# Kernel tuning notes

Hardware: AMD Instinct MI355X
Metric: run time of the kernel (lower is better)

## Reference

```python
import jax, jax.numpy as jnp
import numpy as np

SEQ, B, D_IN, D_H = 4096, 256, 64, 128


def setup_inputs() -> dict:
    key = jax.random.key(0)
    k1, k2, k3, k4, k5 = jax.random.split(key, 5)
    return {
        "input": jax.random.normal(k1, (SEQ, B, D_IN), dtype=jnp.float32),
        "W_ih": jax.random.normal(k2, (D_H, D_IN), dtype=jnp.float32) * (1.0 / np.sqrt(D_IN)),
        "b_ih": jax.random.normal(k3, (D_H,), dtype=jnp.float32) * 0.02,
        "W_hh": jax.random.normal(k4, (D_H, D_H), dtype=jnp.float32) * (1.0 / np.sqrt(D_H)),
        "b_hh": jax.random.normal(k5, (D_H,), dtype=jnp.float32) * 0.02,
    }


def reference(input, W_ih, b_ih, W_hh, b_hh):
    # Precompute input projections for all steps in one big GEMM: [S,B,128]
    x_proj = jnp.einsum('sbi,hi->sbh', input, W_ih) + b_ih + b_hh

    def step(h, x_t):
        # h: [B,128]; tanh(ih(x_t) + hh(h))
        h_new = jnp.tanh(x_t + h @ W_hh.T)
        return h_new, None

    h0 = jnp.zeros((input.shape[1], W_hh.shape[0]), dtype=input.dtype)
    h_final, _ = jax.lax.scan(step, h0, x_proj)
    return h_final  # [B,128]
```

## Files before the change

### kernel.cpp

```cpp
#include <hip/hip_runtime.h>


#define SEQ   4096
#define BATCH 256
#define DIN   64
#define DH    128
#define XSTEP (BATCH * DIN)

typedef _Float16 half8  __attribute__((ext_vector_type(8)));
typedef _Float16 half4v __attribute__((ext_vector_type(4)));
typedef _Float16 half2v __attribute__((ext_vector_type(2)));
typedef __fp16   fp16x2 __attribute__((ext_vector_type(2)));
typedef float    f32x4  __attribute__((ext_vector_type(4)));
typedef float    f32x2  __attribute__((ext_vector_type(2)));

union H2 { fp16x2 q; half2v h; unsigned int u; };

__device__ __forceinline__ float fast_tanh(float v) {
    float e = __builtin_amdgcn_exp2f(v * 2.88539008177792681472f);
    return 1.0f - 2.0f * __builtin_amdgcn_rcpf(e + 1.0f);
}

__device__ __forceinline__ half2v pk(float a, float b) {
    H2 u; u.q = __builtin_amdgcn_cvt_pkrtz(a, b);
    return u.h;
}

__device__ __forceinline__ half8 cvt8(f32x4 a, f32x4 b) {
    half2v p0 = pk(a[0], a[1]);
    half2v p1 = pk(a[2], a[3]);
    half2v p2 = pk(b[0], b[1]);
    half2v p3 = pk(b[2], b[3]);
    half8 r;
    r[0] = p0[0]; r[1] = p0[1]; r[2] = p1[0]; r[3] = p1[1];
    r[4] = p2[0]; r[5] = p2[1]; r[6] = p3[0]; r[7] = p3[1];
    return r;
}

__device__ __forceinline__ half4v pack4(f32x4 a) {
    half2v q0 = pk(a[0], a[1]);
    half2v q1 = pk(a[2], a[3]);
    half4v r;
    r[0] = q0[0]; r[1] = q0[1]; r[2] = q1[0]; r[3] = q1[1];
    return r;
}

__device__ __forceinline__ f32x4 cvt4f(half4v v) {
    f32x4 r;
    r[0] = (float)v[0]; r[1] = (float)v[1];
    r[2] = (float)v[2]; r[3] = (float)v[3];
    return r;
}

__device__ __forceinline__ int hoff(int b, int j) {
    return b * 256 + ((((j >> 3) ^ b) & 15) << 4) + (j & 7) * 2;
}

__launch_bounds__(256, 1)
__global__ void rnn_prepass(const float* __restrict__ x,
                            const float* __restrict__ Wih,
                            const float* __restrict__ bih,
                            const float* __restrict__ bhh,
                            _Float16* __restrict__ xp)
{
    const int tid  = threadIdx.x;
    const int w    = tid >> 6;
    const int lane = tid & 63;
    const int lb   = lane & 15;
    const int lg   = lane >> 4;
    const int rowbase = blockIdx.x * 64 + w * 16;

    half8 A[8][2];
    #pragma unroll
    for (int s = 0; s < 8; ++s) {
        #pragma unroll
        for (int kt = 0; kt < 2; ++kt) {
            const float* wr = Wih + (s * 16 + lb) * DIN + kt * 32 + lg * 8;
            half8 f;
            #pragma unroll
            for (int i = 0; i < 8; ++i) f[i] = (_Float16)wr[i];
            A[s][kt] = f;
        }
    }
    f32x4 bias[8];
    #pragma unroll
    for (int s = 0; s < 8; ++s)
        #pragma unroll
        for (int r = 0; r < 4; ++r) {
            int j = s * 16 + lg * 4 + r;
            bias[s][r] = bih[j] + bhh[j];
        }

    const float* xr = x + (size_t)(rowbase + lb) * DIN + lg * 8;
    half8 xf0 = cvt8(*(const f32x4*)(xr),      *(const f32x4*)(xr + 4));
    half8 xf1 = cvt8(*(const f32x4*)(xr + 32), *(const f32x4*)(xr + 36));

    _Float16* op = xp + (size_t)(rowbase + lb) * DH + lg * 4;
    #pragma unroll
    for (int s = 0; s < 8; ++s) {
        f32x4 acc;
        acc = __builtin_amdgcn_mfma_f32_16x16x32_f16(A[s][0], xf0, bias[s], 0, 0, 0);
        acc = __builtin_amdgcn_mfma_f32_16x16x32_f16(A[s][1], xf1, acc,     0, 0, 0);
        *(half4v*)(op + s * 16) = pack4(acc);
    }
}

__launch_bounds__(512, 1)
__global__ void rnn_scan_xp(const _Float16* __restrict__ xp,
                            const float* __restrict__ Whh,
                            float* __restrict__ out)
{
    __shared__ __align__(16) char hbuf[8192];

    const int tid   = threadIdx.x;
    const int wave  = tid >> 6;
    const int lane  = tid & 63;
    const int lb    = lane & 15;
    const int lg    = lane >> 4;
    const int bbase = blockIdx.x << 4;
    const int jbase = wave << 4;

    half8 Ahh[4];
    #pragma unroll
    for (int kt = 0; kt < 4; ++kt) {
        const float* wr = Whh + (jbase + lb) * DH + kt * 32 + lg * 8;
        half8 f;
        #pragma unroll
        for (int i = 0; i < 8; ++i) f[i] = (_Float16)wr[i];
        Ahh[kt] = f;
    }

    const _Float16* xpp = xp + (size_t)(bbase + lb) * DH + jbase + (lg << 2);
    const size_t XPS = (size_t)BATCH * DH;

    half4v xq1, xq2, xq3;
    f32x4 ci;
    {
        half4v x0 = *(const half4v*)(xpp);
        xq1 = *(const half4v*)(xpp + 1 * XPS);
        xq2 = *(const half4v*)(xpp + 2 * XPS);
        xq3 = *(const half4v*)(xpp + 3 * XPS);
        ci = cvt4f(x0);
    }
    const _Float16* xload = xpp + 4 * XPS;

    half8 hf0, hf1, hf2, hf3;
    {
        half8 z;
        #pragma unroll
        for (int i = 0; i < 8; ++i) z[i] = (_Float16)0.0f;
        hf0 = hf1 = hf2 = hf3 = z;
    }

    const int woff  = hoff(lb, jbase + (lg << 2));
    const int roff0 = hoff(lb, 0 * 32 + (lg << 3));
    const int roff1 = hoff(lb, 1 * 32 + (lg << 3));
    const int roff2 = hoff(lb, 2 * 32 + (lg << 3));
    const int roff3 = hoff(lb, 3 * 32 + (lg << 3));

    #pragma unroll 2
    for (int t = 0; t < SEQ - 1; ++t) {
        const int nb = (t + 1) & 1;
        char* hb = hbuf + nb * 4096;

        f32x4 zz = {0.0f, 0.0f, 0.0f, 0.0f};
        f32x4 acc1, acc2;
        acc1 = __builtin_amdgcn_mfma_f32_16x16x32_f16(Ahh[0], hf0, ci,   0, 0, 0);
        acc2 = __builtin_amdgcn_mfma_f32_16x16x32_f16(Ahh[2], hf2, zz,   0, 0, 0);
        acc1 = __builtin_amdgcn_mfma_f32_16x16x32_f16(Ahh[1], hf1, acc1, 0, 0, 0);
        acc2 = __builtin_amdgcn_mfma_f32_16x16x32_f16(Ahh[3], hf3, acc2, 0, 0, 0);

        half4v xnew = *(const half4v*)xload;
        if (t + 5 < SEQ) xload += XPS;

        f32x4 rA;
        #pragma unroll
        for (int r = 0; r < 4; ++r) rA[r] = fast_tanh(acc1[r] + acc2[r]);
        *(half4v*)(hb + woff) = pack4(rA);

        ci = cvt4f(xq1);
        xq1 = xq2; xq2 = xq3; xq3 = xnew;

        asm volatile("s_waitcnt lgkmcnt(0)" ::: "memory");
        __builtin_amdgcn_s_barrier();
        asm volatile("" ::: "memory");

        hf0 = *(const half8*)(hb + roff0);
        hf2 = *(const half8*)(hb + roff2);
        hf1 = *(const half8*)(hb + roff1);
        hf3 = *(const half8*)(hb + roff3);
    }

    {
        f32x4 zz = {0.0f, 0.0f, 0.0f, 0.0f};
        f32x4 acc1, acc2;
        acc1 = __builtin_amdgcn_mfma_f32_16x16x32_f16(Ahh[0], hf0, ci,   0, 0, 0);
        acc2 = __builtin_amdgcn_mfma_f32_16x16x32_f16(Ahh[2], hf2, zz,   0, 0, 0);
        acc1 = __builtin_amdgcn_mfma_f32_16x16x32_f16(Ahh[1], hf1, acc1, 0, 0, 0);
        acc2 = __builtin_amdgcn_mfma_f32_16x16x32_f16(Ahh[3], hf3, acc2, 0, 0, 0);
        f32x4 rA;
        #pragma unroll
        for (int r = 0; r < 4; ++r) rA[r] = fast_tanh(acc1[r] + acc2[r]);
        *(f32x4*)(out + (size_t)(bbase + lb) * DH + jbase + (lg << 2)) = rA;
    }
}

__device__ __forceinline__ int hoffc(int b, int chunk, int lo) {
    return b * 256 + ((chunk ^ b) << 4) + lo;
}
__device__ __forceinline__ int xoff_lds(int b, int chunk, int lo) {
    return b * 128 + (((chunk ^ (b & 7)) << 4) + lo);
}

__launch_bounds__(512, 1)
__global__ void rnn_fused_scan_r2(const float* __restrict__ x,
                                  const float* __restrict__ Wih,
                                  const float* __restrict__ bih,
                                  const float* __restrict__ Whh,
                                  const float* __restrict__ bhh,
                                  float* __restrict__ out)
{
    __shared__ __align__(16) char lds[12288];
    char* hbuf = lds;
    char* xbuf = lds + 8192;

    const int tid   = threadIdx.x;
    const int wave  = tid >> 6;
    const int lane  = tid & 63;
    const int lb    = lane & 15;
    const int lg    = lane >> 4;
    const int bbase = blockIdx.x << 4;
    const int jbase = wave << 4;

    half8 Ahh[4], Aih[2];
    #pragma unroll
    for (int kt = 0; kt < 4; ++kt) {
        const float* wr = Whh + (jbase + lb) * DH + kt * 32 + lg * 8;
        half8 f;
        #pragma unroll
        for (int i = 0; i < 8; ++i) f[i] = (_Float16)wr[i];
        Ahh[kt] = f;
    }
    #pragma unroll
    for (int kt = 0; kt < 2; ++kt) {
        const float* wr = Wih + (jbase + lb) * DIN + kt * 32 + lg * 8;
        half8 f;
        #pragma unroll
        for (int i = 0; i < 8; ++i) f[i] = (_Float16)wr[i];
        Aih[kt] = f;
    }
    f32x4 bias;
    #pragma unroll
    for (int r = 0; r < 4; ++r) {
        int j = jbase + lg * 4 + r;
        bias[r] = bih[j] + bhh[j];
    }

    const int bx = tid >> 5;
    const int kx = (tid & 31) << 1;
    const float* xlane = x + (size_t)(bbase + bx) * DIN + kx;

    f32x2 r0  = *(const f32x2*)(xlane + 0 * (size_t)XSTEP);
    f32x2 rx0 = *(const f32x2*)(xlane + 1 * (size_t)XSTEP);
    f32x2 rx1 = *(const f32x2*)(xlane + 2 * (size_t)XSTEP);
    f32x2 rx2 = *(const f32x2*)(xlane + 3 * (size_t)XSTEP);
    {
        half2v p; p[0] = (_Float16)r0[0]; p[1] = (_Float16)r0[1];
        *(half2v*)(xbuf + xoff_lds(bx, kx >> 3, (kx & 7) * 2)) = p;
    }
    const float* xload = xlane + 4 * (size_t)XSTEP;

    half8 hf0, hf1, hf2, hf3, xf0, xf1;
    {
        half8 z;
        #pragma unroll
        for (int i = 0; i < 8; ++i) z[i] = (_Float16)0.0f;
        hf0 = hf1 = hf2 = hf3 = z;
    }

    asm volatile("s_waitcnt lgkmcnt(0)" ::: "memory");
    __builtin_amdgcn_s_barrier();
    asm volatile("" ::: "memory");
    xf0 = *(const half8*)(xbuf + xoff_lds(lb, 0 * 4 + lg, 0));
    xf1 = *(const half8*)(xbuf + xoff_lds(lb, 1 * 4 + lg, 0));

    f32x4 acc_ih;
    acc_ih = __builtin_amdgcn_mfma_f32_16x16x32_f16(Aih[0], xf0, bias,   0, 0, 0);
    acc_ih = __builtin_amdgcn_mfma_f32_16x16x32_f16(Aih[1], xf1, acc_ih, 0, 0, 0);

    #pragma unroll 2
    for (int t = 0; t < SEQ - 1; ++t) {
        f32x4 zz = {0.0f, 0.0f, 0.0f, 0.0f};
        f32x4 acc1, acc2;
        acc1 = __builtin_amdgcn_mfma_f32_16x16x32_f16(Ahh[0], hf0, acc_ih, 0, 0, 0);
        acc2 = __builtin_amdgcn_mfma_f32_16x16x32_f16(Ahh[2], hf2, zz,     0, 0, 0);
        acc1 = __builtin_amdgcn_mfma_f32_16x16x32_f16(Ahh[1], hf1, acc1,   0, 0, 0);
        acc2 = __builtin_amdgcn_mfma_f32_16x16x32_f16(Ahh[3], hf3, acc2,   0, 0, 0);

        const int nb = (t + 1) & 1;
        {
            half2v p; p[0] = (_Float16)rx0[0]; p[1] = (_Float16)rx0[1];
            *(half2v*)(xbuf + nb * 2048 + xoff_lds(bx, kx >> 3, (kx & 7) * 2)) = p;
        }
        rx0 = rx1; rx1 = rx2;
        rx2 = *(const f32x2*)xload;
        if (t + 5 < SEQ) xload += XSTEP;

        f32x4 hv;
        #pragma unroll
        for (int r = 0; r < 4; ++r) hv[r] = fast_tanh(acc1[r] + acc2[r]);
        {
            half4v p;
            #pragma unroll
            for (int r = 0; r < 4; ++r) p[r] = (_Float16)hv[r];
            *(half4v*)(hbuf + nb * 4096 + hoffc(lb, (wave << 1) + (lg >> 1), (lg & 1) * 8)) = p;
        }

        asm volatile("s_waitcnt lgkmcnt(0)" ::: "memory");
        __builtin_amdgcn_s_barrier();
        asm volatile("" ::: "memory");

        hf0 = *(const half8*)(hbuf + nb * 4096 + hoffc(lb, 0 * 4 + lg, 0));
        hf2 = *(const half8*)(hbuf + nb * 4096 + hoffc(lb, 2 * 4 + lg, 0));
        hf1 = *(const half8*)(hbuf + nb * 4096 + hoffc(lb, 1 * 4 + lg, 0));
        hf3 = *(const half8*)(hbuf + nb * 4096 + hoffc(lb, 3 * 4 + lg, 0));
        xf0 = *(const half8*)(xbuf + nb * 2048 + xoff_lds(lb, 0 * 4 + lg, 0));
        xf1 = *(const half8*)(xbuf + nb * 2048 + xoff_lds(lb, 1 * 4 + lg, 0));

        acc_ih = __builtin_amdgcn_mfma_f32_16x16x32_f16(Aih[0], xf0, bias,   0, 0, 0);
        acc_ih = __builtin_amdgcn_mfma_f32_16x16x32_f16(Aih[1], xf1, acc_ih, 0, 0, 0);
    }

    {
        f32x4 zz = {0.0f, 0.0f, 0.0f, 0.0f};
        f32x4 acc1, acc2;
        acc1 = __builtin_amdgcn_mfma_f32_16x16x32_f16(Ahh[0], hf0, acc_ih, 0, 0, 0);
        acc2 = __builtin_amdgcn_mfma_f32_16x16x32_f16(Ahh[2], hf2, zz,     0, 0, 0);
        acc1 = __builtin_amdgcn_mfma_f32_16x16x32_f16(Ahh[1], hf1, acc1,   0, 0, 0);
        acc2 = __builtin_amdgcn_mfma_f32_16x16x32_f16(Ahh[3], hf3, acc2,   0, 0, 0);
        f32x4 res;
        #pragma unroll
        for (int r = 0; r < 4; ++r) res[r] = fast_tanh(acc1[r] + acc2[r]);
        *(f32x4*)(out + (size_t)(bbase + lb) * DH + jbase + (lg << 2)) = res;
    }
}

extern "C" void kernel_launch(void* const* d_in, const int* in_sizes, int n_in,
                              void* d_out, int out_size, void* d_ws, size_t ws_size,
                              hipStream_t stream) {
    const float* x   = (const float*)d_in[0];
    const float* Wih = (const float*)d_in[1];
    const float* bih = (const float*)d_in[2];
    const float* Whh = (const float*)d_in[3];
    const float* bhh = (const float*)d_in[4];
    float* out = (float*)d_out;

    const size_t need = (size_t)SEQ * BATCH * DH * sizeof(_Float16);
    if (ws_size >= need) {
        _Float16* xp = (_Float16*)d_ws;
        rnn_prepass<<<SEQ * BATCH / 64, 256, 0, stream>>>(x, Wih, bih, bhh, xp);
        rnn_scan_xp<<<16, 512, 0, stream>>>(xp, Whh, out);
    } else {
        rnn_fused_scan_r2<<<16, 512, 0, stream>>>(x, Wih, bih, Whh, bhh, out);
    }
}
```

Baseline: 1.424 ms.

## Fuse input projection into scan with producer waves and per-block global ring

Replaces the separate prepass GEMM kernel plus scan kernel with one kernel of 768 threads per block. Four low-priority producer waves compute the input projection 64 steps ahead into a per-block global ring buffer, and eight high-priority consumer waves run the recurrence, reading x_proj from the ring. This removes the full-size intermediate write/read and the second launch, and overlaps projection work with the latency-bound scan. The cost is that every timestep now carries a block-wide barrier shared with the producers. Ring visibility relies on barriers and vmcnt waits rather than explicit fences.

```diff
diff --git a/kernel.cpp b/kernel.cpp
--- a/kernel.cpp
+++ b/kernel.cpp
@@ -5,7 +5,10 @@
 #define BATCH 256
 #define DIN   64
 #define DH    128
-#define XSTEP (BATCH * DIN)
+#define LEAD   64
+#define RSLOTS 128
+#define SLOT_BYTES 4096
+#define RING_BYTES ((size_t)RSLOTS * SLOT_BYTES)
 
 typedef _Float16 half8  __attribute__((ext_vector_type(8)));
 typedef _Float16 half4v __attribute__((ext_vector_type(4)));
@@ -19,6 +22,10 @@
 __device__ __forceinline__ float fast_tanh(float v) {
     float e = __builtin_amdgcn_exp2f(v * 2.88539008177792681472f);
     return 1.0f - 2.0f * __builtin_amdgcn_rcpf(e + 1.0f);
+}
+
+__device__ __forceinline__ int hoff(int b, int j) {
+    return b * 256 + ((((j >> 3) ^ b) & 15) << 4) + (j & 7) * 2;
 }
 
 __device__ __forceinline__ half2v pk(float a, float b) {
@@ -52,63 +59,23 @@
     return r;
 }
 
-__device__ __forceinline__ int hoff(int b, int j) {
-    return b * 256 + ((((j >> 3) ^ b) & 15) << 4) + (j & 7) * 2;
-}
-
-__launch_bounds__(256, 1)
-__global__ void rnn_prepass(const float* __restrict__ x,
-                            const float* __restrict__ Wih,
-                            const float* __restrict__ bih,
-                            const float* __restrict__ bhh,
-                            _Float16* __restrict__ xp)
-{
-    const int tid  = threadIdx.x;
-    const int w    = tid >> 6;
-    const int lane = tid & 63;
-    const int lb   = lane & 15;
-    const int lg   = lane >> 4;
-    const int rowbase = blockIdx.x * 64 + w * 16;
-
-    half8 A[8][2];
-    #pragma unroll
-    for (int s = 0; s < 8; ++s) {
-        #pragma unroll
-        for (int kt = 0; kt < 2; ++kt) {
-            const float* wr = Wih + (s * 16 + lb) * DIN + kt * 32 + lg * 8;
-            half8 f;
-            #pragma unroll
-            for (int i = 0; i < 8; ++i) f[i] = (_Float16)wr[i];
-            A[s][kt] = f;
-        }
-    }
-    f32x4 bias[8];
-    #pragma unroll
-    for (int s = 0; s < 8; ++s)
-        #pragma unroll
-        for (int r = 0; r < 4; ++r) {
-            int j = s * 16 + lg * 4 + r;
-            bias[s][r] = bih[j] + bhh[j];
-        }
-
-    const float* xr = x + (size_t)(rowbase + lb) * DIN + lg * 8;
-    half8 xf0 = cvt8(*(const f32x4*)(xr),      *(const f32x4*)(xr + 4));
-    half8 xf1 = cvt8(*(const f32x4*)(xr + 32), *(const f32x4*)(xr + 36));
-
-    _Float16* op = xp + (size_t)(rowbase + lb) * DH + lg * 4;
-    #pragma unroll
-    for (int s = 0; s < 8; ++s) {
-        f32x4 acc;
-        acc = __builtin_amdgcn_mfma_f32_16x16x32_f16(A[s][0], xf0, bias[s], 0, 0, 0);
-        acc = __builtin_amdgcn_mfma_f32_16x16x32_f16(A[s][1], xf1, acc,     0, 0, 0);
-        *(half4v*)(op + s * 16) = pack4(acc);
-    }
-}
-
-__launch_bounds__(512, 1)
-__global__ void rnn_scan_xp(const _Float16* __restrict__ xp,
-                            const float* __restrict__ Whh,
-                            float* __restrict__ out)
+struct XSlot { f32x4 v0, v1, v2, v3; };
+
+#define XLOAD(slot, p_) do {                                           \
+        (slot).v0 = *(const f32x4*)(p_);                               \
+        (slot).v1 = *(const f32x4*)((p_) + 4);                         \
+        (slot).v2 = *(const f32x4*)((p_) + 32);                        \
+        (slot).v3 = *(const f32x4*)((p_) + 36);                        \
+    } while (0)
+
+__launch_bounds__(768, 3)
+__global__ void rnn_fused_all(const float* __restrict__ x,
+                              const float* __restrict__ Wih,
+                              const float* __restrict__ bih,
+                              const float* __restrict__ Whh,
+                              const float* __restrict__ bhh,
+                              float* __restrict__ out,
+                              char* __restrict__ ring_all)
 {
     __shared__ __align__(16) char hbuf[8192];
 
@@ -118,93 +85,147 @@
     const int lb    = lane & 15;
     const int lg    = lane >> 4;
     const int bbase = blockIdx.x << 4;
-    const int jbase = wave << 4;
-
-    half8 Ahh[4];
-    #pragma unroll
-    for (int kt = 0; kt < 4; ++kt) {
-        const float* wr = Whh + (jbase + lb) * DH + kt * 32 + lg * 8;
-        half8 f;
-        #pragma unroll
-        for (int i = 0; i < 8; ++i) f[i] = (_Float16)wr[i];
-        Ahh[kt] = f;
-    }
-
-    const _Float16* xpp = xp + (size_t)(bbase + lb) * DH + jbase + (lg << 2);
-    const size_t XPS = (size_t)BATCH * DH;
-
-    half4v xq1, xq2, xq3;
-    f32x4 ci;
-    {
-        half4v x0 = *(const half4v*)(xpp);
-        xq1 = *(const half4v*)(xpp + 1 * XPS);
-        xq2 = *(const half4v*)(xpp + 2 * XPS);
-        xq3 = *(const half4v*)(xpp + 3 * XPS);
-        ci = cvt4f(x0);
-    }
-    const _Float16* xload = xpp + 4 * XPS;
-
-    half8 hf0, hf1, hf2, hf3;
-    {
-        half8 z;
-        #pragma unroll
-        for (int i = 0; i < 8; ++i) z[i] = (_Float16)0.0f;
-        hf0 = hf1 = hf2 = hf3 = z;
-    }
-
-    const int woff  = hoff(lb, jbase + (lg << 2));
-    const int roff0 = hoff(lb, 0 * 32 + (lg << 3));
-    const int roff1 = hoff(lb, 1 * 32 + (lg << 3));
-    const int roff2 = hoff(lb, 2 * 32 + (lg << 3));
-    const int roff3 = hoff(lb, 3 * 32 + (lg << 3));
-
-    #pragma unroll 2
-    for (int t = 0; t < SEQ - 1; ++t) {
-        const int nb = (t + 1) & 1;
-        char* hb = hbuf + nb * 4096;
-
-        f32x4 zz = {0.0f, 0.0f, 0.0f, 0.0f};
-        f32x4 acc1, acc2;
-        acc1 = __builtin_amdgcn_mfma_f32_16x16x32_f16(Ahh[0], hf0, ci,   0, 0, 0);
-        acc2 = __builtin_amdgcn_mfma_f32_16x16x32_f16(Ahh[2], hf2, zz,   0, 0, 0);
-        acc1 = __builtin_amdgcn_mfma_f32_16x16x32_f16(Ahh[1], hf1, acc1, 0, 0, 0);
-        acc2 = __builtin_amdgcn_mfma_f32_16x16x32_f16(Ahh[3], hf3, acc2, 0, 0, 0);
-
-        half4v xnew = *(const half4v*)xload;
-        if (t + 5 < SEQ) xload += XPS;
-
-        f32x4 rA;
-        #pragma unroll
-        for (int r = 0; r < 4; ++r) rA[r] = fast_tanh(acc1[r] + acc2[r]);
-        *(half4v*)(hb + woff) = pack4(rA);
-
-        ci = cvt4f(xq1);
-        xq1 = xq2; xq2 = xq3; xq3 = xnew;
-
-        asm volatile("s_waitcnt lgkmcnt(0)" ::: "memory");
-        __builtin_amdgcn_s_barrier();
-        asm volatile("" ::: "memory");
-
-        hf0 = *(const half8*)(hb + roff0);
-        hf2 = *(const half8*)(hb + roff2);
-        hf1 = *(const half8*)(hb + roff1);
-        hf3 = *(const half8*)(hb + roff3);
-    }
-
-    {
-        f32x4 zz = {0.0f, 0.0f, 0.0f, 0.0f};
-        f32x4 acc1, acc2;
-        acc1 = __builtin_amdgcn_mfma_f32_16x16x32_f16(Ahh[0], hf0, ci,   0, 0, 0);
-        acc2 = __builtin_amdgcn_mfma_f32_16x16x32_f16(Ahh[2], hf2, zz,   0, 0, 0);
-        acc1 = __builtin_amdgcn_mfma_f32_16x16x32_f16(Ahh[1], hf1, acc1, 0, 0, 0);
-        acc2 = __builtin_amdgcn_mfma_f32_16x16x32_f16(Ahh[3], hf3, acc2, 0, 0, 0);
-        f32x4 rA;
-        #pragma unroll
-        for (int r = 0; r < 4; ++r) rA[r] = fast_tanh(acc1[r] + acc2[r]);
-        *(f32x4*)(out + (size_t)(bbase + lb) * DH + jbase + (lg << 2)) = rA;
-    }
-}
-
+    char* ring = ring_all + (size_t)blockIdx.x * RING_BYTES;
+
+    if (wave < 8) {
+        __builtin_amdgcn_s_setprio(1);
+        const int jbase = wave << 4;
+
+        half8 Ahh[4];
+        #pragma unroll
+        for (int kt = 0; kt < 4; ++kt) {
+            const float* wr = Whh + (jbase + lb) * DH + kt * 32 + (lg << 3);
+            half8 f;
+            #pragma unroll
+            for (int i = 0; i < 8; ++i) f[i] = (_Float16)wr[i];
+            Ahh[kt] = f;
+        }
+        f32x4 biasv;
+        #pragma unroll
+        for (int r = 0; r < 4; ++r) {
+            int j = jbase + (lg << 2) + r;
+            biasv[r] = bih[j] + bhh[j];
+        }
+
+        const int woff  = hoff(lb, jbase + (lg << 2));
+        const int roff0 = hoff(lb, 0 * 32 + (lg << 3));
+        const int roff1 = hoff(lb, 1 * 32 + (lg << 3));
+        const int roff2 = hoff(lb, 2 * 32 + (lg << 3));
+        const int roff3 = hoff(lb, 3 * 32 + (lg << 3));
+        const int rdoff = lb * 256 + ((jbase + (lg << 2)) << 1);
+
+        half8 hf0, hf1, hf2, hf3;
+        {
+            half8 z;
+            #pragma unroll
+            for (int i = 0; i < 8; ++i) z[i] = (_Float16)0.0f;
+            hf0 = hf1 = hf2 = hf3 = z;
+        }
+        f32x4 ci = {0.0f, 0.0f, 0.0f, 0.0f};
+        half4v xq1 = {};
+
+        #pragma unroll 2
+        for (int s = -LEAD; s < SEQ - 1; ++s) {
+            if (s >= 0) {
+                const int t = s;
+                char* hb = hbuf + (((t + 1) & 1) << 12);
+
+                f32x4 zz = {0.0f, 0.0f, 0.0f, 0.0f};
+                f32x4 acc1, acc2;
+                acc1 = __builtin_amdgcn_mfma_f32_16x16x32_f16(Ahh[0], hf0, ci,   0, 0, 0);
+                acc2 = __builtin_amdgcn_mfma_f32_16x16x32_f16(Ahh[2], hf2, zz,   0, 0, 0);
+                acc1 = __builtin_amdgcn_mfma_f32_16x16x32_f16(Ahh[1], hf1, acc1, 0, 0, 0);
+                acc2 = __builtin_amdgcn_mfma_f32_16x16x32_f16(Ahh[3], hf3, acc2, 0, 0, 0);
+
+                const int tn = (t + 2 < SEQ) ? t + 2 : SEQ - 1;
+                half4v xnew = *(const half4v*)(ring + ((tn & (RSLOTS - 1)) * SLOT_BYTES) + rdoff);
+
+                f32x4 rA;
+                #pragma unroll
+                for (int r = 0; r < 4; ++r) rA[r] = fast_tanh(acc1[r] + acc2[r]);
+                *(half4v*)(hb + woff) = pack4(rA);
+
+                ci = cvt4f(xq1) + biasv;
+                xq1 = xnew;
+
+                asm volatile("s_waitcnt lgkmcnt(0)" ::: "memory");
+                __builtin_amdgcn_s_barrier();
+                asm volatile("" ::: "memory");
+
+                hf0 = *(const half8*)(hb + roff0);
+                hf2 = *(const half8*)(hb + roff2);
+                hf1 = *(const half8*)(hb + roff1);
+                hf3 = *(const half8*)(hb + roff3);
+            } else {
+                __builtin_amdgcn_s_barrier();
+                asm volatile("" ::: "memory");
+                if (s == -1) {
+                    half4v x0 = *(const half4v*)(ring + 0 * SLOT_BYTES + rdoff);
+                    xq1       = *(const half4v*)(ring + 1 * SLOT_BYTES + rdoff);
+                    ci = cvt4f(x0) + biasv;
+                }
+            }
+        }
+
+        {
+            f32x4 zz = {0.0f, 0.0f, 0.0f, 0.0f};
+            f32x4 acc1, acc2;
+            acc1 = __builtin_amdgcn_mfma_f32_16x16x32_f16(Ahh[0], hf0, ci,   0, 0, 0);
+            acc2 = __builtin_amdgcn_mfma_f32_16x16x32_f16(Ahh[2], hf2, zz,   0, 0, 0);
+            acc1 = __builtin_amdgcn_mfma_f32_16x16x32_f16(Ahh[1], hf1, acc1, 0, 0, 0);
+            acc2 = __builtin_amdgcn_mfma_f32_16x16x32_f16(Ahh[3], hf3, acc2, 0, 0, 0);
+            f32x4 rA;
+            #pragma unroll
+            for (int r = 0; r < 4; ++r) rA[r] = fast_tanh(acc1[r] + acc2[r]);
+            *(f32x4*)(out + (size_t)(bbase + lb) * DH + jbase + (lg << 2)) = rA;
+        }
+    } else {
+        __builtin_amdgcn_s_setprio(0);
+        const int h = wave - 8;
+
+        half8 Aih[8][2];
+        #pragma unroll
+        for (int s8 = 0; s8 < 8; ++s8) {
+            #pragma unroll
+            for (int kt = 0; kt < 2; ++kt) {
+                const float* wr = Wih + (s8 * 16 + lb) * DIN + kt * 32 + (lg << 3);
+                half8 f;
+                #pragma unroll
+                for (int i = 0; i < 8; ++i) f[i] = (_Float16)wr[i];
+                Aih[s8][kt] = f;
+            }
+        }
+
+        XSlot xs;
+        XLOAD(xs, x + ((size_t)h * BATCH + bbase + lb) * DIN + (lg << 3));
+
+        for (int s = -LEAD; s < SEQ - 1; ++s) {
+            const int tp = s + LEAD;
+            if ((tp & 3) == h && tp < SEQ) {
+                half8 xf0 = cvt8(xs.v0, xs.v1);
+                half8 xf1 = cvt8(xs.v2, xs.v3);
+                char* wp = ring + ((tp & (RSLOTS - 1)) * SLOT_BYTES) + lb * 256 + (lg << 3);
+                f32x4 zz = {0.0f, 0.0f, 0.0f, 0.0f};
+                #pragma unroll
+                for (int s8 = 0; s8 < 8; ++s8) {
+                    f32x4 a;
+                    a = __builtin_amdgcn_mfma_f32_16x16x32_f16(Aih[s8][0], xf0, zz, 0, 0, 0);
+                    a = __builtin_amdgcn_mfma_f32_16x16x32_f16(Aih[s8][1], xf1, a,  0, 0, 0);
+                    *(half4v*)(wp + s8 * 32) = pack4(a);
+                }
+                const int tl = tp + 4;
+                if (tl < SEQ) {
+                    XLOAD(xs, x + ((size_t)tl * BATCH + bbase + lb) * DIN + (lg << 3));
+                }
+                asm volatile("s_waitcnt vmcnt(4)" ::: "memory");
+            }
+            __builtin_amdgcn_s_barrier();
+            asm volatile("" ::: "memory");
+        }
+    }
+}
+
+#define XSTEP (BATCH * DIN)
 __device__ __forceinline__ int hoffc(int b, int chunk, int lo) {
     return b * 256 + ((chunk ^ b) << 4) + lo;
 }
@@ -355,11 +376,9 @@
     const float* bhh = (const float*)d_in[4];
     float* out = (float*)d_out;
 
-    const size_t need = (size_t)SEQ * BATCH * DH * sizeof(_Float16);
+    const size_t need = 16 * RING_BYTES;
     if (ws_size >= need) {
-        _Float16* xp = (_Float16*)d_ws;
-        rnn_prepass<<<SEQ * BATCH / 64, 256, 0, stream>>>(x, Wih, bih, bhh, xp);
-        rnn_scan_xp<<<16, 512, 0, stream>>>(xp, Whh, out);
+        rnn_fused_all<<<16, 768, 0, stream>>>(x, Wih, bih, Whh, bhh, out, (char*)d_ws);
     } else {
         rnn_fused_scan_r2<<<16, 512, 0, stream>>>(x, Wih, bih, Whh, bhh, out);
     }
```

New measurement: 2.765 ms. 94.1% more time.

## Overlap input projection with recurrent scan via producer-consumer persistent kernel

Applied to the files above, without the earlier changes.

Replaces the separate prepass and scan launches with one 80-block kernel. Sixteen blocks run the recurrent scan, and 64 producer blocks compute the fp16 input projection per batch group. Producers publish progress through atomic ready counters that consumers poll before each 32-step chunk. This hides the projection GEMM time behind the serial scan. In exchange it adds a memset launch, polling overhead, and depends on producer and consumer blocks being co-resident to avoid deadlock.

```diff
diff --git a/kernel.cpp b/kernel.cpp
--- a/kernel.cpp
+++ b/kernel.cpp
@@ -6,6 +6,7 @@
 #define DIN   64
 #define DH    128
 #define XSTEP (BATCH * DIN)
+#define XP_BYTES ((size_t)SEQ * BATCH * DH * 2)
 
 typedef _Float16 half8  __attribute__((ext_vector_type(8)));
 typedef _Float16 half4v __attribute__((ext_vector_type(4)));
@@ -56,7 +57,206 @@
     return b * 256 + ((((j >> 3) ^ b) & 15) << 4) + (j & 7) * 2;
 }
 
-__launch_bounds__(256, 1)
+struct XSlot { f32x4 v0, v1, v2, v3; };
+#define XLOAD(slot, p_) do {                                           \
+        (slot).v0 = *(const f32x4*)(p_);                               \
+        (slot).v1 = *(const f32x4*)((p_) + 4);                         \
+        (slot).v2 = *(const f32x4*)((p_) + 32);                        \
+        (slot).v3 = *(const f32x4*)((p_) + 36);                        \
+    } while (0)
+
+__device__ __forceinline__ void pollwait(const int* rdy, int tgt) {
+    for (;;) {
+        int r0 = __hip_atomic_load(rdy + 0, __ATOMIC_ACQUIRE, __HIP_MEMORY_SCOPE_AGENT);
+        int r1 = __hip_atomic_load(rdy + 1, __ATOMIC_ACQUIRE, __HIP_MEMORY_SCOPE_AGENT);
+        int r2 = __hip_atomic_load(rdy + 2, __ATOMIC_ACQUIRE, __HIP_MEMORY_SCOPE_AGENT);
+        int r3 = __hip_atomic_load(rdy + 3, __ATOMIC_ACQUIRE, __HIP_MEMORY_SCOPE_AGENT);
+        int m = r0 < r1 ? r0 : r1;
+        int n = r2 < r3 ? r2 : r3;
+        if (n < m) m = n;
+        if (4 * m >= tgt) return;
+        __builtin_amdgcn_s_sleep(8);
+    }
+}
+
+__launch_bounds__(512, 1)
+__global__ void rnn_pc(const float* __restrict__ x,
+                       const float* __restrict__ Wih,
+                       const float* __restrict__ bih,
+                       const float* __restrict__ Whh,
+                       const float* __restrict__ bhh,
+                       float* __restrict__ out,
+                       _Float16* __restrict__ xp,
+                       int* __restrict__ ready)
+{
+    __shared__ __align__(16) char hbuf[8192];
+
+    const int tid  = threadIdx.x;
+    const int wave = tid >> 6;
+    const int lane = tid & 63;
+    const int lb   = lane & 15;
+    const int lg   = lane >> 4;
+
+    if (blockIdx.x < 16) {
+        const int g     = blockIdx.x;
+        const int bbase = g << 4;
+        const int jbase = wave << 4;
+        const int* rdy  = ready + g * 4;
+
+        half8 Ahh[4];
+        #pragma unroll
+        for (int kt = 0; kt < 4; ++kt) {
+            const float* wr = Whh + (jbase + lb) * DH + kt * 32 + (lg << 3);
+            half8 f;
+            #pragma unroll
+            for (int i = 0; i < 8; ++i) f[i] = (_Float16)wr[i];
+            Ahh[kt] = f;
+        }
+
+        pollwait(rdy, 8);
+
+        const _Float16* xpp = xp + (size_t)(bbase + lb) * DH + jbase + (lg << 2);
+        const size_t XPS = (size_t)BATCH * DH;
+
+        half4v xq1, xq2, xq3;
+        f32x4 ci;
+        {
+            half4v x0 = *(const half4v*)(xpp);
+            xq1 = *(const half4v*)(xpp + 1 * XPS);
+            xq2 = *(const half4v*)(xpp + 2 * XPS);
+            xq3 = *(const half4v*)(xpp + 3 * XPS);
+            ci = cvt4f(x0);
+        }
+        const _Float16* xload = xpp + 4 * XPS;
+
+        half8 hf0, hf1, hf2, hf3;
+        {
+            half8 z;
+            #pragma unroll
+            for (int i = 0; i < 8; ++i) z[i] = (_Float16)0.0f;
+            hf0 = hf1 = hf2 = hf3 = z;
+        }
+
+        const int woff  = hoff(lb, jbase + (lg << 2));
+        const int roff0 = hoff(lb, 0 * 32 + (lg << 3));
+        const int roff1 = hoff(lb, 1 * 32 + (lg << 3));
+        const int roff2 = hoff(lb, 2 * 32 + (lg << 3));
+        const int roff3 = hoff(lb, 3 * 32 + (lg << 3));
+
+        #define SCAN_BODY(T_) do {                                                   \
+            const int t_ = (T_);                                                     \
+            char* hb = hbuf + (((t_ + 1) & 1) << 12);                                \
+            f32x4 zz = {0.0f, 0.0f, 0.0f, 0.0f};                                     \
+            f32x4 acc1, acc2;                                                        \
+            acc1 = __builtin_amdgcn_mfma_f32_16x16x32_f16(Ahh[0], hf0, ci,   0,0,0); \
+            acc2 = __builtin_amdgcn_mfma_f32_16x16x32_f16(Ahh[2], hf2, zz,   0,0,0); \
+            acc1 = __builtin_amdgcn_mfma_f32_16x16x32_f16(Ahh[1], hf1, acc1, 0,0,0); \
+            acc2 = __builtin_amdgcn_mfma_f32_16x16x32_f16(Ahh[3], hf3, acc2, 0,0,0); \
+            half4v xnew = *(const half4v*)xload;                                     \
+            if (t_ + 5 < SEQ) xload += XPS;                                          \
+            f32x4 rA;                                                                \
+            _Pragma("unroll")                                                        \
+            for (int r = 0; r < 4; ++r) rA[r] = fast_tanh(acc1[r] + acc2[r]);        \
+            *(half4v*)(hb + woff) = pack4(rA);                                       \
+            ci = cvt4f(xq1);                                                         \
+            xq1 = xq2; xq2 = xq3; xq3 = xnew;                                        \
+            asm volatile("s_waitcnt lgkmcnt(0)" ::: "memory");                       \
+            __builtin_amdgcn_s_barrier();                                            \
+            asm volatile("" ::: "memory");                                           \
+            hf0 = *(const half8*)(hb + roff0);                                       \
+            hf2 = *(const half8*)(hb + roff2);                                       \
+            hf1 = *(const half8*)(hb + roff1);                                       \
+            hf3 = *(const half8*)(hb + roff3);                                       \
+        } while (0)
+
+        for (int T = 0; T < 4064; T += 32) {
+            pollwait(rdy, T + 36);
+            #pragma unroll 2
+            for (int tt = 0; tt < 32; ++tt) SCAN_BODY(T + tt);
+        }
+        pollwait(rdy, 4096);
+        #pragma unroll 2
+        for (int t = 4064; t < 4095; ++t) SCAN_BODY(t);
+
+        {
+            f32x4 zz = {0.0f, 0.0f, 0.0f, 0.0f};
+            f32x4 acc1, acc2;
+            acc1 = __builtin_amdgcn_mfma_f32_16x16x32_f16(Ahh[0], hf0, ci,   0, 0, 0);
+            acc2 = __builtin_amdgcn_mfma_f32_16x16x32_f16(Ahh[2], hf2, zz,   0, 0, 0);
+            acc1 = __builtin_amdgcn_mfma_f32_16x16x32_f16(Ahh[1], hf1, acc1, 0, 0, 0);
+            acc2 = __builtin_amdgcn_mfma_f32_16x16x32_f16(Ahh[3], hf3, acc2, 0, 0, 0);
+            f32x4 rA;
+            #pragma unroll
+            for (int r = 0; r < 4; ++r) rA[r] = fast_tanh(acc1[r] + acc2[r]);
+            *(f32x4*)(out + (size_t)(bbase + lb) * DH + jbase + (lg << 2)) = rA;
+        }
+        #undef SCAN_BODY
+    } else {
+        const int p  = blockIdx.x - 16;
+        const int g  = p >> 2;
+        const int q  = p & 3;
+        const int bb = g << 4;
+
+        half8 A[8][2];
+        #pragma unroll
+        for (int s = 0; s < 8; ++s) {
+            #pragma unroll
+            for (int kt = 0; kt < 2; ++kt) {
+                const float* wr = Wih + (s * 16 + lb) * DIN + kt * 32 + (lg << 3);
+                half8 f;
+                #pragma unroll
+                for (int i = 0; i < 8; ++i) f[i] = (_Float16)wr[i];
+                A[s][kt] = f;
+            }
+        }
+        f32x4 bias[8];
+        #pragma unroll
+        for (int s = 0; s < 8; ++s)
+            #pragma unroll
+            for (int r = 0; r < 4; ++r) {
+                int j = s * 16 + (lg << 2) + r;
+                bias[s][r] = bih[j] + bhh[j];
+            }
+
+        XSlot xs;
+        {
+            int t0 = q + (wave << 2);
+            XLOAD(xs, x + ((size_t)t0 * BATCH + bb + lb) * DIN + (lg << 3));
+        }
+
+        for (int i = 0; i < 128; ++i) {
+            const int t = q + ((((i << 3) + wave)) << 2);
+
+            half8 xf0 = cvt8(xs.v0, xs.v1);
+            half8 xf1 = cvt8(xs.v2, xs.v3);
+
+            XSlot xn;
+            if (i + 1 < 128) {
+                int tn = q + (((((i + 1) << 3) + wave)) << 2);
+                XLOAD(xn, x + ((size_t)tn * BATCH + bb + lb) * DIN + (lg << 3));
+            }
+
+            _Float16* op = xp + ((size_t)t * BATCH + bb + lb) * DH + (lg << 2);
+            #pragma unroll
+            for (int s = 0; s < 8; ++s) {
+                f32x4 acc;
+                acc = __builtin_amdgcn_mfma_f32_16x16x32_f16(A[s][0], xf0, bias[s], 0, 0, 0);
+                acc = __builtin_amdgcn_mfma_f32_16x16x32_f16(A[s][1], xf1, acc,     0, 0, 0);
+                *(half4v*)(op + s * 16) = pack4(acc);
+            }
+            if (i + 1 < 128) xs = xn;
+
+            __syncthreads();
+
+            if (tid == 0 && (i < 8 || (i & 3) == 3)) {
+                __hip_atomic_store(&ready[g * 4 + q], 8 * (i + 1),
+                                   __ATOMIC_RELEASE, __HIP_MEMORY_SCOPE_AGENT);
+            }
+        }
+    }
+}
+
+__launch_bounds__(256)
 __global__ void rnn_prepass(const float* __restrict__ x,
                             const float* __restrict__ Wih,
                             const float* __restrict__ bih,
@@ -72,7 +272,7 @@
 
     half8 A[8][2];
     #pragma unroll
-    for (int s = 0; s < 8; ++s) {
+    for (int s = 0; s < 8; ++s)
         #pragma unroll
         for (int kt = 0; kt < 2; ++kt) {
             const float* wr = Wih + (s * 16 + lb) * DIN + kt * 32 + lg * 8;
@@ -81,7 +281,6 @@
             for (int i = 0; i < 8; ++i) f[i] = (_Float16)wr[i];
             A[s][kt] = f;
         }
-    }
     f32x4 bias[8];
     #pragma unroll
     for (int s = 0; s < 8; ++s)
@@ -355,8 +554,12 @@
     const float* bhh = (const float*)d_in[4];
     float* out = (float*)d_out;
 
-    const size_t need = (size_t)SEQ * BATCH * DH * sizeof(_Float16);
-    if (ws_size >= need) {
+    if (ws_size >= XP_BYTES + 4096) {
+        _Float16* xp = (_Float16*)d_ws;
+        int* ready = (int*)((char*)d_ws + XP_BYTES);
+        hipMemsetAsync(ready, 0, 4096, stream);
+        rnn_pc<<<80, 512, 0, stream>>>(x, Wih, bih, Whh, bhh, out, xp, ready);
+    } else if (ws_size >= XP_BYTES) {
         _Float16* xp = (_Float16*)d_ws;
         rnn_prepass<<<SEQ * BATCH / 64, 256, 0, stream>>>(x, Wih, bih, bhh, xp);
         rnn_scan_xp<<<16, 512, 0, stream>>>(xp, Whh, out);
```

Measured after the change: 2.207 ms. +55.0%, slower.
